# Kernel optimization log

Measured on AMD Instinct MI355X. Metric: run time of the kernel, lower is better.

Reference implementation:

```python
import jax, jax.numpy as jnp
import numpy as np

B, S, D = 2, 2048, 4096
N_Q_HEADS, N_KV_HEADS, HEAD_DIM = 32, 8, 128
N_REP = N_Q_HEADS // N_KV_HEADS
ROPE_THETA = 10000.0


def setup_inputs() -> dict:
    key = jax.random.key(0)
    ks = jax.random.split(key, 5)
    x = jax.random.normal(ks[0], (B, S, D), dtype=jnp.float32)
    sc = 1.0 / np.sqrt(D)
    wq = jax.random.normal(ks[1], (D, N_Q_HEADS * HEAD_DIM), dtype=jnp.float32) * sc
    wk = jax.random.normal(ks[2], (D, N_KV_HEADS * HEAD_DIM), dtype=jnp.float32) * sc
    wv = jax.random.normal(ks[3], (D, N_KV_HEADS * HEAD_DIM), dtype=jnp.float32) * sc
    cache_k = jnp.zeros((B, S, N_KV_HEADS, HEAD_DIM), dtype=jnp.float32)
    cache_v = jnp.zeros((B, S, N_KV_HEADS, HEAD_DIM), dtype=jnp.float32)
    # rotary frequencies: theta_i = 1/ROPE_THETA^(2i/hd), angle = pos * theta_i
    inv_freq = 1.0 / (ROPE_THETA ** (np.arange(0, HEAD_DIM, 2, dtype=np.float32) / HEAD_DIM))
    angles = np.arange(S, dtype=np.float32)[:, None] * inv_freq[None, :]  # [S, hd/2]
    freqs_cos = jnp.asarray(np.cos(angles), dtype=jnp.float32)
    freqs_sin = jnp.asarray(np.sin(angles), dtype=jnp.float32)
    return {"x": x, "wq": wq, "wk": wk, "wv": wv,
            "cache_k": cache_k, "cache_v": cache_v,
            "freqs_cos": freqs_cos, "freqs_sin": freqs_sin,
            "start_pos": 0}


def _apply_rope(x, cos, sin):
    # x: [B, S, H, hd]; cos/sin: [S, hd/2] -> complex rotation of adjacent pairs
    xr = x[..., 0::2]
    xi = x[..., 1::2]
    c = cos[None, :, None, :]
    s = sin[None, :, None, :]
    out_r = xr * c - xi * s
    out_i = xr * s + xi * c
    return jnp.stack([out_r, out_i], axis=-1).reshape(x.shape)


def reference(x, wq, wk, wv, cache_k, cache_v, freqs_cos, freqs_sin, start_pos):
    batch, seq_len, _ = x.shape
    xq = (x @ wq).reshape(batch, seq_len, N_Q_HEADS, HEAD_DIM)
    xk = (x @ wk).reshape(batch, seq_len, N_KV_HEADS, HEAD_DIM)
    xv = (x @ wv).reshape(batch, seq_len, N_KV_HEADS, HEAD_DIM)
    xq = _apply_rope(xq, freqs_cos, freqs_sin)
    xk = _apply_rope(xk, freqs_cos, freqs_sin)
    # KV-cache append
    cache_k = jax.lax.dynamic_update_slice(cache_k, xk, (0, start_pos, 0, 0))
    cache_v = jax.lax.dynamic_update_slice(cache_v, xv, (0, start_pos, 0, 0))
    keys = cache_k[:, : start_pos + seq_len]    # [B, T, Hkv, hd]
    values = cache_v[:, : start_pos + seq_len]
    # GQA: repeat kv heads to match query heads
    keys = jnp.repeat(keys, N_REP, axis=2)      # [B, T, Hq, hd]
    values = jnp.repeat(values, N_REP, axis=2)
    scale = 1.0 / jnp.sqrt(jnp.asarray(HEAD_DIM, dtype=x.dtype))
    scores = jnp.einsum("bqhd,bkhd->bhqk", xq, keys) * scale
    probs = jax.nn.softmax(scores.astype(jnp.float32), axis=-1).astype(xq.dtype)
    out = jnp.einsum("bhqk,bkhd->bqhd", probs, values)
    return out.reshape(batch, seq_len, N_Q_HEADS * HEAD_DIM)
```

## Files before the change

### kernel.cpp

```cpp
#include <hip/hip_runtime.h>

#define BATCH   2
#define S_LEN   2048
#define D_MODEL 4096
#define HD      128
#define NQH     32
#define NKVH    8

typedef unsigned short ushort_t;
typedef __bf16 bf16x8 __attribute__((ext_vector_type(8)));
typedef float floatx4 __attribute__((ext_vector_type(4)));

#define MFMA16(a, b, c) __builtin_amdgcn_mfma_f32_16x16x32_bf16(a, b, c, 0, 0, 0)

#if __has_builtin(__builtin_amdgcn_exp2f)
#define EXP2(x) __builtin_amdgcn_exp2f(x)
#else
#define EXP2(x) __expf((x) * 0.6931471805599453f)
#endif

__device__ __forceinline__ ushort_t f2b(float f) {
    unsigned int x;
    __builtin_memcpy(&x, &f, 4);
    x += 0x7fff + ((x >> 16) & 1);
    return (ushort_t)(x >> 16);
}

__device__ __forceinline__ void gld16(void* lds, const void* g) {
    __builtin_amdgcn_global_load_lds(
        (const __attribute__((address_space(1))) void*)g,
        (__attribute__((address_space(3))) void*)lds, 16, 0, 0);
}

__global__ __launch_bounds__(256) void conv_x(const float* __restrict__ x,
                                              ushort_t* __restrict__ x0,
                                              ushort_t* __restrict__ x1) {
    const size_t i = ((size_t)blockIdx.x * 256 + threadIdx.x) << 2;
    float4 v = *(const float4*)&x[i];
    ushort4 p;
    p.x = f2b(v.x); p.y = f2b(v.y); p.z = f2b(v.z); p.w = f2b(v.w);
    ushort_t* dst = (i < 8388608) ? x0 : x1;
    *(ushort4*)&dst[i & 8388607] = p;
}

__global__ __launch_bounds__(256) void pack_w(const float* __restrict__ wq,
                                              const float* __restrict__ wk,
                                              const float* __restrict__ wv,
                                              ushort_t* __restrict__ WT) {
    __shared__ ushort_t t[64][65];
    const int k0 = blockIdx.x << 6;
    const int n0 = blockIdx.y << 6;
    const float* src;
    int scol, sN;
    if (n0 < 4096)      { src = wq; scol = n0;        sN = 4096; }
    else if (n0 < 5120) { src = wk; scol = n0 - 4096; sN = 1024; }
    else                { src = wv; scol = n0 - 5120; sN = 1024; }
    const int tid = threadIdx.x;
#pragma unroll
    for (int i = 0; i < 16; i++) {
        int idx = tid + (i << 8);
        int r = idx >> 6, c = idx & 63;
        t[r][c] = f2b(src[(size_t)(k0 + r) * sN + scol + c]);
    }
    __syncthreads();
#pragma unroll
    for (int i = 0; i < 16; i++) {
        int idx = tid + (i << 8);
        int r = idx >> 6, c = idx & 63;
        WT[(size_t)(n0 + r) * D_MODEL + k0 + c] = t[c][r];
    }
}

__global__ __launch_bounds__(512, 2) void gemm_qkv(const ushort_t* __restrict__ x0,
                                                   const ushort_t* __restrict__ x1,
                                                   const ushort_t* __restrict__ WT,
                                                   const float* __restrict__ fc,
                                                   const float* __restrict__ fs,
                                                   ushort_t* __restrict__ Qr,
                                                   ushort_t* __restrict__ Kr,
                                                   ushort_t* __restrict__ Vt) {
    __shared__ ushort_t At[2][256 * 64];
    __shared__ ushort_t Bt[2][256 * 64];

    const int tid  = threadIdx.x;
    const int wid  = tid >> 6;
    const int lane = tid & 63;
    const int wm = (wid >> 2) << 7;
    const int wn = (wid & 3) << 6;
    const int bm = blockIdx.y << 8;
    const int bn = blockIdx.x << 8;
    const int cl = lane & 15, rg = lane >> 4, l7 = lane & 7;

    const ushort_t* Xb = (bm < 2048) ? x0 : x1;
    const int bml = bm & 2047;

    const int srow8 = tid >> 3;
    const int gsw   = (tid & 7) ^ (srow8 & 7);
    const ushort_t* gA = Xb + (size_t)(bml + srow8) * D_MODEL + (gsw << 3);
    const ushort_t* gB = WT + (size_t)(bn  + srow8) * D_MODEL + (gsw << 3);
    const int lbase = (wid << 3) << 6;

    floatx4 acc[8][4] = {};
    bf16x8 af[4][2], bfr[4][2];

    auto stA = [&](int buf, int t, int half) {
#pragma unroll
        for (int j = 0; j < 2; j++) {
            const int row0 = (half << 7) + (j << 6);
            gld16(&At[buf][(row0 << 6) + lbase],
                  gA + (size_t)row0 * D_MODEL + ((size_t)t << 6));
        }
    };
    auto stB = [&](int buf, int t, int half) {
#pragma unroll
        for (int j = 0; j < 2; j++) {
            const int row0 = (half << 7) + (j << 6);
            gld16(&Bt[buf][(row0 << 6) + lbase],
                  gB + (size_t)row0 * D_MODEL + ((size_t)t << 6));
        }
    };
    auto loadA = [&](const ushort_t* buf, int mh) {
#pragma unroll
        for (int i = 0; i < 4; i++) {
            const int row = wm + (mh << 6) + (i << 4) + cl;
#pragma unroll
            for (int kk = 0; kk < 2; kk++)
                af[i][kk] = *(const bf16x8*)
                    &buf[(row << 6) + ((((kk << 2) + rg) ^ l7) << 3)];
        }
    };
    auto loadB = [&](const ushort_t* buf) {
#pragma unroll
        for (int i = 0; i < 4; i++) {
            const int row = wn + (i << 4) + cl;
#pragma unroll
            for (int kk = 0; kk < 2; kk++)
                bfr[i][kk] = *(const bf16x8*)
                    &buf[(row << 6) + ((((kk << 2) + rg) ^ l7) << 3)];
        }
    };

    stA(0, 0, 0); stA(0, 0, 1); stB(0, 0, 0); stB(0, 0, 1);

#pragma unroll 1
    for (int t = 0; t < 64; t++) {
        const int d = t & 1, e = d ^ 1;
        const ushort_t* Ad = At[d];
        const ushort_t* Bd = Bt[d];

        if (t < 63) {
            stA(e, t + 1, 0); stA(e, t + 1, 1);
            asm volatile("s_waitcnt vmcnt(4)" ::: "memory");
        } else {
            asm volatile("s_waitcnt vmcnt(0)" ::: "memory");
        }
        __builtin_amdgcn_s_barrier();
        asm volatile("" ::: "memory");
        loadA(Ad, 0);
        loadB(Bd);
        __builtin_amdgcn_s_setprio(1);
#pragma unroll
        for (int i = 0; i < 4; i++)
#pragma unroll
            for (int j = 0; j < 2; j++)
#pragma unroll
                for (int kk = 0; kk < 2; kk++)
                    acc[i][j] = MFMA16(af[i][kk], bfr[j][kk], acc[i][j]);
        __builtin_amdgcn_s_setprio(0);
        asm volatile("" ::: "memory");
        __builtin_amdgcn_s_barrier();

        if (t < 63) stB(e, t + 1, 0);
        __builtin_amdgcn_s_setprio(1);
#pragma unroll
        for (int i = 0; i < 4; i++)
#pragma unroll
            for (int j = 0; j < 2; j++)
#pragma unroll
                for (int kk = 0; kk < 2; kk++)
                    acc[i][2 + j] = MFMA16(af[i][kk], bfr[2 + j][kk], acc[i][2 + j]);
        __builtin_amdgcn_s_setprio(0);
        asm volatile("" ::: "memory");
        __builtin_amdgcn_s_barrier();

        if (t < 63) stB(e, t + 1, 1);
        loadA(Ad, 1);
        __builtin_amdgcn_s_setprio(1);
#pragma unroll
        for (int i = 0; i < 4; i++)
#pragma unroll
            for (int j = 0; j < 2; j++)
#pragma unroll
                for (int kk = 0; kk < 2; kk++)
                    acc[4 + i][j] = MFMA16(af[i][kk], bfr[j][kk], acc[4 + i][j]);
        __builtin_amdgcn_s_setprio(0);
        asm volatile("" ::: "memory");
        __builtin_amdgcn_s_barrier();

        __builtin_amdgcn_s_setprio(1);
#pragma unroll
        for (int i = 0; i < 4; i++)
#pragma unroll
            for (int j = 0; j < 2; j++)
#pragma unroll
                for (int kk = 0; kk < 2; kk++)
                    acc[4 + i][2 + j] = MFMA16(af[i][kk], bfr[2 + j][kk], acc[4 + i][2 + j]);
        __builtin_amdgcn_s_setprio(0);
        asm volatile("" ::: "memory");
        __builtin_amdgcn_s_barrier();
    }

    const int b_idx  = bm >> 11;
    const int s_base = (bm & 2047) + wm;
    const int col0   = bn + wn;
    const int dbase  = col0 & 127;

    if (col0 < 5120) {
        const float oscale = (col0 < 4096)
            ? (0.08838834764831845f * 1.4426950408889634f) : 1.0f;
        ushort_t* dst = (col0 < 4096)
            ? Qr + (size_t)(b_idx * NQH  + (col0 >> 7)) * S_LEN * HD
            : Kr + (size_t)(b_idx * NKVH + ((col0 - 4096) >> 7)) * S_LEN * HD;
#pragma unroll
        for (int fn = 0; fn < 4; fn++) {
            const int dcol = dbase + (fn << 4) + cl;
            const int d2   = dcol >> 1;
            const float sgn = (dcol & 1) ? 1.0f : -1.0f;
#pragma unroll
            for (int fm = 0; fm < 8; fm++)
#pragma unroll
                for (int r = 0; r < 4; r++) {
                    float v  = acc[fm][fn][r];
                    float pv = __shfl_xor(v, 1);
                    int srow = s_base + (fm << 4) + (rg << 2) + r;
                    float c  = fc[(srow << 6) + d2];
                    float s  = fs[(srow << 6) + d2];
                    float o  = (v * c + sgn * pv * s) * oscale;
                    dst[(size_t)srow * HD + dcol] = f2b(o);
                }
        }
    } else {
        const int kvh = (col0 - 5120) >> 7;
        ushort_t* dst = Vt + (size_t)(b_idx * NKVH + kvh) * HD * S_LEN;
#pragma unroll
        for (int fm = 0; fm < 8; fm++) {
            const int srow = s_base + (fm << 4) + (rg << 2);
#pragma unroll
            for (int fn = 0; fn < 4; fn++) {
                const int dcol = dbase + (fn << 4) + cl;
                ushort4 pk;
                pk.x = f2b(acc[fm][fn][0]);
                pk.y = f2b(acc[fm][fn][1]);
                pk.z = f2b(acc[fm][fn][2]);
                pk.w = f2b(acc[fm][fn][3]);
                *(ushort4*)&dst[(size_t)dcol * S_LEN + srow] = pk;
            }
        }
    }
}

__global__ __launch_bounds__(256, 3) void attn(const ushort_t* __restrict__ Qr,
                                               const ushort_t* __restrict__ Kr,
                                               const ushort_t* __restrict__ Vtg,
                                               float* __restrict__ out) {
    __shared__ ushort_t Ktb[2][32 * 128];
    __shared__ ushort_t Vlb[2][128 * 32];
    __shared__ ushort_t Pt[4 * 32 * 40];

    const int tid  = threadIdx.x;
    const int wid  = tid >> 6;
    const int lane = tid & 63;
    const int h  = blockIdx.y;
    const int b  = blockIdx.z;
    const int kh = h >> 2;
    const int q0 = (blockIdx.x << 7) + (wid << 5);

    const int cl = lane & 15, rg = lane >> 4, l7 = lane & 7;

    const ushort_t* Qbase = Qr + ((size_t)(b * NQH + h) * S_LEN + q0 + cl) * HD;
    bf16x8 qf0[4], qf1[4];
#pragma unroll
    for (int dc = 0; dc < 4; dc++) {
        qf0[dc] = *(const bf16x8*)&Qbase[(dc << 5) + (rg << 3)];
        qf1[dc] = *(const bf16x8*)&Qbase[(size_t)16 * HD + (dc << 5) + (rg << 3)];
    }

    floatx4 o0[8] = {}, o1[8] = {};
    float ls0[4] = {0.f, 0.f, 0.f, 0.f};
    float ls1[4] = {0.f, 0.f, 0.f, 0.f};

    const ushort_t* Kb = Kr  + (size_t)(b * NKVH + kh) * S_LEN * HD;
    const ushort_t* Vb = Vtg + (size_t)(b * NKVH + kh) * HD * S_LEN;
    ushort_t* Pw = &Pt[wid * 32 * 40];

    const int vr  = lane >> 2;
    const int gv2 = (lane & 3) ^ (vr & 3);

    auto stage = [&](int bi, int kt0) {
#pragma unroll
        for (int i = 0; i < 2; i++) {
            int ki = (wid << 1) + i;
            gld16(&Ktb[bi][ki << 9],
                  Kb + (size_t)(kt0 + (ki << 2) + rg) * HD
                     + ((cl ^ (((ki & 1) << 2) + rg)) << 3));
            gld16(&Vlb[bi][ki << 9],
                  Vb + (size_t)((ki << 4) + vr) * S_LEN + kt0 + (gv2 << 3));
        }
    };

    stage(0, 0);

#pragma unroll 1
    for (int t = 0; t < 64; t++) {
        if (t < 63) {
            stage((t + 1) & 1, (t + 1) << 5);
            asm volatile("s_waitcnt vmcnt(4)" ::: "memory");
        } else {
            asm volatile("s_waitcnt vmcnt(0)" ::: "memory");
        }
        __builtin_amdgcn_s_barrier();
        asm volatile("" ::: "memory");

        const ushort_t* Kc = Ktb[t & 1];
        const ushort_t* Vc = Vlb[t & 1];

        __builtin_amdgcn_s_setprio(1);
#pragma unroll
        for (int kt = 0; kt < 2; kt++) {
            floatx4 a0 = {0.f, 0.f, 0.f, 0.f};
            floatx4 a1 = {0.f, 0.f, 0.f, 0.f};
#pragma unroll
            for (int dc = 0; dc < 4; dc++) {
                int c = (dc << 2) + rg;
                bf16x8 kf = *(const bf16x8*)
                    &Kc[(((kt << 4) + cl) << 7) + ((c ^ l7) << 3)];
                a0 = MFMA16(qf0[dc], kf, a0);
                a1 = MFMA16(qf1[dc], kf, a1);
            }
#pragma unroll
            for (int r = 0; r < 4; r++) {
                float p0 = EXP2(a0[r]);
                float p1 = EXP2(a1[r]);
                ls0[r] += p0;
                ls1[r] += p1;
                Pw[(((rg << 2) + r)     ) * 40 + (kt << 4) + cl] = f2b(p0);
                Pw[(((rg << 2) + r) + 16) * 40 + (kt << 4) + cl] = f2b(p1);
            }
        }

        {
            bf16x8 pf0 = *(const bf16x8*)&Pw[ cl       * 40 + (rg << 3)];
            bf16x8 pf1 = *(const bf16x8*)&Pw[(cl + 16) * 40 + (rg << 3)];
#pragma unroll
            for (int dt = 0; dt < 8; dt++) {
                int d = (dt << 4) + cl;
                bf16x8 vf = *(const bf16x8*)
                    &Vc[(d << 5) + ((rg ^ (cl & 3)) << 3)];
                o0[dt] = MFMA16(pf0, vf, o0[dt]);
                o1[dt] = MFMA16(pf1, vf, o1[dt]);
            }
        }
        __builtin_amdgcn_s_setprio(0);

        asm volatile("" ::: "memory");
        __builtin_amdgcn_s_barrier();
    }

#pragma unroll
    for (int r = 0; r < 4; r++) {
        float v0 = ls0[r];
        v0 += __shfl_xor(v0, 1);
        v0 += __shfl_xor(v0, 2);
        v0 += __shfl_xor(v0, 4);
        v0 += __shfl_xor(v0, 8);
        ls0[r] = 1.0f / v0;
        float v1 = ls1[r];
        v1 += __shfl_xor(v1, 1);
        v1 += __shfl_xor(v1, 2);
        v1 += __shfl_xor(v1, 4);
        v1 += __shfl_xor(v1, 8);
        ls1[r] = 1.0f / v1;
    }

    float* ob = out + (size_t)(b * S_LEN + q0) * (NQH * HD) + h * HD;
#pragma unroll
    for (int dt = 0; dt < 8; dt++)
#pragma unroll
        for (int r = 0; r < 4; r++) {
            ob[(size_t)((rg << 2) + r) * (NQH * HD) + (dt << 4) + cl] =
                o0[dt][r] * ls0[r];
            ob[(size_t)((rg << 2) + r + 16) * (NQH * HD) + (dt << 4) + cl] =
                o1[dt][r] * ls1[r];
        }
}

extern "C" void kernel_launch(void* const* d_in, const int* in_sizes, int n_in,
                              void* d_out, int out_size, void* d_ws, size_t ws_size,
                              hipStream_t stream) {
    const float* x  = (const float*)d_in[0];
    const float* wq = (const float*)d_in[1];
    const float* wk = (const float*)d_in[2];
    const float* wv = (const float*)d_in[3];
    ushort_t* x0 = (ushort_t*)d_in[4];
    ushort_t* x1 = (ushort_t*)d_in[5];
    const float* fc = (const float*)d_in[6];
    const float* fs = (const float*)d_in[7];
    float* out = (float*)d_out;

    ushort_t* WTx = (ushort_t*)d_in[0];

    char* ws = (char*)d_ws;
    ushort_t* Qr = (ushort_t*)(ws);
    ushort_t* Kr = (ushort_t*)(ws + 33554432);
    ushort_t* Vt = (ushort_t*)(ws + 41943040);

    conv_x  <<<16384,           256, 0, stream>>>(x, x0, x1);
    pack_w  <<<dim3(64, 96),    256, 0, stream>>>(wq, wk, wv, WTx);
    gemm_qkv<<<dim3(24, 16),    512, 0, stream>>>(x0, x1, WTx, fc, fs, Qr, Kr, Vt);
    attn    <<<dim3(16, 32, 2), 256, 0, stream>>>(Qr, Kr, Vt, out);
    (void)in_sizes; (void)n_in; (void)out_size; (void)ws_size;
}
```

Baseline: 650.0 us.

## Shrink QKV GEMM tile to 256x128 and restructure prefetch into two-stage pipeline

The QKV projection GEMM tile drops from 256x256 to 256x128, which doubles the grid to 768 blocks for better CU fill on the 256-CU part. The main loop is restructured so each tile issues half of the next tile's loads early and the following tile's loads after the first MFMA half. Each region maps to one 128-wide head. The smaller tile raises A-matrix reload traffic, and the reduced LDS footprint may allow more resident blocks.

```diff
diff --git a/kernel.cpp b/kernel.cpp
--- a/kernel.cpp
+++ b/kernel.cpp
@@ -80,15 +80,15 @@
                                                    ushort_t* __restrict__ Kr,
                                                    ushort_t* __restrict__ Vt) {
     __shared__ ushort_t At[2][256 * 64];
-    __shared__ ushort_t Bt[2][256 * 64];
+    __shared__ ushort_t Bt[2][128 * 64];
 
     const int tid  = threadIdx.x;
     const int wid  = tid >> 6;
     const int lane = tid & 63;
     const int wm = (wid >> 2) << 7;
-    const int wn = (wid & 3) << 6;
+    const int wn = (wid & 3) << 5;
     const int bm = blockIdx.y << 8;
-    const int bn = blockIdx.x << 8;
+    const int bn = blockIdx.x << 7;
     const int cl = lane & 15, rg = lane >> 4, l7 = lane & 7;
 
     const ushort_t* Xb = (bm < 2048) ? x0 : x1;
@@ -100,29 +100,21 @@
     const ushort_t* gB = WT + (size_t)(bn  + srow8) * D_MODEL + (gsw << 3);
     const int lbase = (wid << 3) << 6;
 
-    floatx4 acc[8][4] = {};
-    bf16x8 af[4][2], bfr[4][2];
-
-    auto stA = [&](int buf, int t, int half) {
-#pragma unroll
-        for (int j = 0; j < 2; j++) {
-            const int row0 = (half << 7) + (j << 6);
-            gld16(&At[buf][(row0 << 6) + lbase],
-                  gA + (size_t)row0 * D_MODEL + ((size_t)t << 6));
-        }
-    };
-    auto stB = [&](int buf, int t, int half) {
-#pragma unroll
-        for (int j = 0; j < 2; j++) {
-            const int row0 = (half << 7) + (j << 6);
-            gld16(&Bt[buf][(row0 << 6) + lbase],
-                  gB + (size_t)row0 * D_MODEL + ((size_t)t << 6));
-        }
-    };
-    auto loadA = [&](const ushort_t* buf, int mh) {
+    floatx4 acc[8][2] = {};
+    bf16x8 af[4][2], bf[2][2];
+
+    auto stA = [&](int d, int T, int u) {
+        gld16(&At[d][((u << 6) << 6) + lbase],
+              gA + (size_t)(u << 6) * D_MODEL + ((size_t)T << 6));
+    };
+    auto stB = [&](int d, int T, int u) {
+        gld16(&Bt[d][((u << 6) << 6) + lbase],
+              gB + (size_t)(u << 6) * D_MODEL + ((size_t)T << 6));
+    };
+    auto loadA = [&](const ushort_t* buf, int half) {
 #pragma unroll
         for (int i = 0; i < 4; i++) {
-            const int row = wm + (mh << 6) + (i << 4) + cl;
+            const int row = wm + (half << 6) + (i << 4) + cl;
 #pragma unroll
             for (int kk = 0; kk < 2; kk++)
                 af[i][kk] = *(const bf16x8*)
@@ -131,33 +123,44 @@
     };
     auto loadB = [&](const ushort_t* buf) {
 #pragma unroll
-        for (int i = 0; i < 4; i++) {
-            const int row = wn + (i << 4) + cl;
+        for (int j = 0; j < 2; j++) {
+            const int row = wn + (j << 4) + cl;
 #pragma unroll
             for (int kk = 0; kk < 2; kk++)
-                bfr[i][kk] = *(const bf16x8*)
+                bf[j][kk] = *(const bf16x8*)
                     &buf[(row << 6) + ((((kk << 2) + rg) ^ l7) << 3)];
         }
     };
 
-    stA(0, 0, 0); stA(0, 0, 1); stB(0, 0, 0); stB(0, 0, 1);
-
-#pragma unroll 1
-    for (int t = 0; t < 64; t++) {
-        const int d = t & 1, e = d ^ 1;
+    auto do_tile = [&](int d, int T) {
         const ushort_t* Ad = At[d];
         const ushort_t* Bd = Bt[d];
-
-        if (t < 63) {
-            stA(e, t + 1, 0); stA(e, t + 1, 1);
-            asm volatile("s_waitcnt vmcnt(4)" ::: "memory");
+        loadA(Ad, 0);
+        loadB(Bd);
+        if (T + 1 < 64) { stA(d ^ 1, T + 1, 1); stA(d ^ 1, T + 1, 3); stB(d ^ 1, T + 1, 1); }
+        asm volatile("" ::: "memory");
+        __builtin_amdgcn_s_barrier();
+        asm volatile("" ::: "memory");
+        __builtin_amdgcn_s_setprio(1);
+#pragma unroll
+        for (int i = 0; i < 4; i++)
+#pragma unroll
+            for (int j = 0; j < 2; j++)
+#pragma unroll
+                for (int kk = 0; kk < 2; kk++)
+                    acc[i][j] = MFMA16(af[i][kk], bf[j][kk], acc[i][j]);
+        __builtin_amdgcn_s_setprio(0);
+        asm volatile("" ::: "memory");
+        __builtin_amdgcn_s_barrier();
+        loadA(Ad, 1);
+        if (T + 2 < 64) {
+            stA(d, T + 2, 0); stA(d, T + 2, 2); stB(d, T + 2, 0);
+            asm volatile("s_waitcnt vmcnt(3)" ::: "memory");
         } else {
             asm volatile("s_waitcnt vmcnt(0)" ::: "memory");
         }
         __builtin_amdgcn_s_barrier();
         asm volatile("" ::: "memory");
-        loadA(Ad, 0);
-        loadB(Bd);
         __builtin_amdgcn_s_setprio(1);
 #pragma unroll
         for (int i = 0; i < 4; i++)
@@ -165,65 +168,38 @@
             for (int j = 0; j < 2; j++)
 #pragma unroll
                 for (int kk = 0; kk < 2; kk++)
-                    acc[i][j] = MFMA16(af[i][kk], bfr[j][kk], acc[i][j]);
+                    acc[4 + i][j] = MFMA16(af[i][kk], bf[j][kk], acc[4 + i][j]);
         __builtin_amdgcn_s_setprio(0);
         asm volatile("" ::: "memory");
         __builtin_amdgcn_s_barrier();
-
-        if (t < 63) stB(e, t + 1, 0);
-        __builtin_amdgcn_s_setprio(1);
-#pragma unroll
-        for (int i = 0; i < 4; i++)
-#pragma unroll
-            for (int j = 0; j < 2; j++)
-#pragma unroll
-                for (int kk = 0; kk < 2; kk++)
-                    acc[i][2 + j] = MFMA16(af[i][kk], bfr[2 + j][kk], acc[i][2 + j]);
-        __builtin_amdgcn_s_setprio(0);
-        asm volatile("" ::: "memory");
-        __builtin_amdgcn_s_barrier();
-
-        if (t < 63) stB(e, t + 1, 1);
-        loadA(Ad, 1);
-        __builtin_amdgcn_s_setprio(1);
-#pragma unroll
-        for (int i = 0; i < 4; i++)
-#pragma unroll
-            for (int j = 0; j < 2; j++)
-#pragma unroll
-                for (int kk = 0; kk < 2; kk++)
-                    acc[4 + i][j] = MFMA16(af[i][kk], bfr[j][kk], acc[4 + i][j]);
-        __builtin_amdgcn_s_setprio(0);
-        asm volatile("" ::: "memory");
-        __builtin_amdgcn_s_barrier();
-
-        __builtin_amdgcn_s_setprio(1);
-#pragma unroll
-        for (int i = 0; i < 4; i++)
-#pragma unroll
-            for (int j = 0; j < 2; j++)
-#pragma unroll
-                for (int kk = 0; kk < 2; kk++)
-                    acc[4 + i][2 + j] = MFMA16(af[i][kk], bfr[2 + j][kk], acc[4 + i][2 + j]);
-        __builtin_amdgcn_s_setprio(0);
-        asm volatile("" ::: "memory");
-        __builtin_amdgcn_s_barrier();
-    }
-
+    };
+
+    stA(0, 0, 0); stA(0, 0, 1); stA(0, 0, 2); stA(0, 0, 3);
+    stB(0, 0, 0); stB(0, 0, 1);
+    stA(1, 1, 0); stA(1, 1, 2); stB(1, 1, 0);
+    asm volatile("s_waitcnt vmcnt(3)" ::: "memory");
+    __builtin_amdgcn_s_barrier();
+    asm volatile("" ::: "memory");
+
+#pragma unroll 1
+    for (int t = 0; t < 64; t += 2) {
+        do_tile(0, t);
+        do_tile(1, t + 1);
+    }
+
+    const int region = blockIdx.x;
     const int b_idx  = bm >> 11;
     const int s_base = (bm & 2047) + wm;
-    const int col0   = bn + wn;
-    const int dbase  = col0 & 127;
-
-    if (col0 < 5120) {
-        const float oscale = (col0 < 4096)
+
+    if (region < 40) {
+        const float oscale = (region < 32)
             ? (0.08838834764831845f * 1.4426950408889634f) : 1.0f;
-        ushort_t* dst = (col0 < 4096)
-            ? Qr + (size_t)(b_idx * NQH  + (col0 >> 7)) * S_LEN * HD
-            : Kr + (size_t)(b_idx * NKVH + ((col0 - 4096) >> 7)) * S_LEN * HD;
-#pragma unroll
-        for (int fn = 0; fn < 4; fn++) {
-            const int dcol = dbase + (fn << 4) + cl;
+        ushort_t* dst = (region < 32)
+            ? Qr + (size_t)(b_idx * NQH  +  region      ) * S_LEN * HD
+            : Kr + (size_t)(b_idx * NKVH + (region - 32)) * S_LEN * HD;
+#pragma unroll
+        for (int fn = 0; fn < 2; fn++) {
+            const int dcol = wn + (fn << 4) + cl;
             const int d2   = dcol >> 1;
             const float sgn = (dcol & 1) ? 1.0f : -1.0f;
 #pragma unroll
@@ -240,14 +216,14 @@
                 }
         }
     } else {
-        const int kvh = (col0 - 5120) >> 7;
+        const int kvh = region - 40;
         ushort_t* dst = Vt + (size_t)(b_idx * NKVH + kvh) * HD * S_LEN;
 #pragma unroll
         for (int fm = 0; fm < 8; fm++) {
             const int srow = s_base + (fm << 4) + (rg << 2);
 #pragma unroll
-            for (int fn = 0; fn < 4; fn++) {
-                const int dcol = dbase + (fn << 4) + cl;
+            for (int fn = 0; fn < 2; fn++) {
+                const int dcol = wn + (fn << 4) + cl;
                 ushort4 pk;
                 pk.x = f2b(acc[fm][fn][0]);
                 pk.y = f2b(acc[fm][fn][1]);
@@ -416,7 +392,7 @@
 
     conv_x  <<<16384,           256, 0, stream>>>(x, x0, x1);
     pack_w  <<<dim3(64, 96),    256, 0, stream>>>(wq, wk, wv, WTx);
-    gemm_qkv<<<dim3(24, 16),    512, 0, stream>>>(x0, x1, WTx, fc, fs, Qr, Kr, Vt);
+    gemm_qkv<<<dim3(48, 16),    512, 0, stream>>>(x0, x1, WTx, fc, fs, Qr, Kr, Vt);
     attn    <<<dim3(16, 32, 2), 256, 0, stream>>>(Qr, Kr, Vt, out);
     (void)in_sizes; (void)n_in; (void)out_size; (void)ws_size;
 }
```

Measured after the change: 619.8 us. 1.05x faster.
